# Kernel tuning notes

Measured on AMD Instinct MI355X. Metric: run time of the kernel, lower is better.

The kernel has to match this reference:

```python
import jax, jax.numpy as jnp
import numpy as np

B, T, NB, H = 1024, 128, 13, 128
T_IN = 64  # input_timesteps


def setup_inputs() -> dict:
    key = jax.random.key(0)
    ks = jax.random.split(key, 7)
    s = 1.0 / np.sqrt(H)
    return {
        "x": jax.random.normal(ks[0], (B, T, NB), dtype=jnp.float32),
        "W_ih": jax.random.normal(ks[1], (4 * H, NB), dtype=jnp.float32) * s,
        "W_hh": jax.random.normal(ks[2], (4 * H, H), dtype=jnp.float32) * s,
        "b_ih": jax.random.normal(ks[3], (4 * H,), dtype=jnp.float32) * s,
        "b_hh": jax.random.normal(ks[4], (4 * H,), dtype=jnp.float32) * s,
        "W_out": jax.random.normal(ks[5], (NB, H), dtype=jnp.float32) * s,
        "b_out": jax.random.normal(ks[6], (NB,), dtype=jnp.float32) * s,
    }


def _lstm_cell(x_t, h, c, W_ih, W_hh, b_ih, b_hh):
    # PyTorch nn.LSTM gate order: input, forget, cell(g), output
    gates = x_t @ W_ih.T + h @ W_hh.T + (b_ih + b_hh)  # [B, 4H]
    i, f, g, o = jnp.split(gates, 4, axis=-1)
    i = jax.nn.sigmoid(i)
    f = jax.nn.sigmoid(f)
    g = jnp.tanh(g)
    o = jax.nn.sigmoid(o)
    c_new = f * c + i * g
    h_new = o * jnp.tanh(c_new)
    return h_new, c_new


def reference(x, W_ih, W_hh, b_ih, b_hh, W_out, b_out):
    # forward_train with teacher_forcing=False, gp_enabled=False:
    # 1) teacher-fed LSTM over x[:, :T_IN]
    batch = x.shape[0]
    h0 = jnp.zeros((batch, H), dtype=x.dtype)
    c0 = jnp.zeros((batch, H), dtype=x.dtype)

    def step_teacher(carry, x_t):
        h, c = carry
        h, c = _lstm_cell(x_t, h, c, W_ih, W_hh, b_ih, b_hh)
        y = h @ W_out.T + b_out  # [B, NB]
        return (h, c), y

    (h, c), ys1 = jax.lax.scan(step_teacher, (h0, c0),
                               jnp.swapaxes(x[:, :T_IN], 0, 1))  # ys1: [T_IN, B, NB]

    remaining = T - T_IN - 1

    def step_auto(carry, _):
        h, c, inp = carry
        h, c = _lstm_cell(inp, h, c, W_ih, W_hh, b_ih, b_hh)
        y = h @ W_out.T + b_out
        return (h, c, y), y

    _, ys2 = jax.lax.scan(step_auto, (h, c, x[:, T_IN]), None, length=remaining)

    out = jnp.concatenate([
        x[:, 0:1],
        jnp.swapaxes(ys1, 0, 1),
        jnp.swapaxes(ys2, 0, 1),
    ], axis=1)  # [B, T, NB]
    return out
```

## Files before the change

### kernel.cpp

```cpp
#include <hip/hip_runtime.h>
#include <math.h>

#define BATCH 1024
#define TT    128
#define NBI   13
#define HH    128
#define T_INP 64
#define BB    16
#define NBLK  (BATCH/BB)

#define LOG2E 1.4426950408889634f

typedef _Float16 half8 __attribute__((ext_vector_type(8)));
typedef _Float16 half4 __attribute__((ext_vector_type(4)));
typedef float    f32x4 __attribute__((ext_vector_type(4)));

__device__ __forceinline__ unsigned short f16b(float v) {
    return __builtin_bit_cast(unsigned short, (_Float16)v);
}
__device__ __forceinline__ float rcpf_(float x) { return __builtin_amdgcn_rcpf(x); }

#if __has_builtin(__builtin_amdgcn_exp2f)
__device__ __forceinline__ float exp2_(float x) { return __builtin_amdgcn_exp2f(x); }
#else
__device__ __forceinline__ float exp2_(float x) { return __expf(x * 0.6931471805599453f); }
#endif

__device__ __forceinline__ void barrier_lds() {
    asm volatile("s_waitcnt lgkmcnt(0)" ::: "memory");
    __builtin_amdgcn_sched_barrier(0);
    __builtin_amdgcn_s_barrier();
    __builtin_amdgcn_sched_barrier(0);
}

#define WS_WHH   0
#define WS_WHAT  131072
#define WS_WIHP  262144
#define WS_WOUT  294912
#define WS_BT    299008
#define WS_BA    301056

__global__ void fold_kernel(const float* __restrict__ W_ih,
                            const float* __restrict__ W_hh,
                            const float* __restrict__ b_ih,
                            const float* __restrict__ b_hh,
                            const float* __restrict__ W_out,
                            const float* __restrict__ b_out,
                            unsigned char* __restrict__ ws)
{
    const int j = blockIdx.x;
    const int k = threadIdx.x;
    unsigned short* whh16  = (unsigned short*)(ws + WS_WHH);
    unsigned short* what16 = (unsigned short*)(ws + WS_WHAT);
    unsigned short* wihp16 = (unsigned short*)(ws + WS_WIHP);
    unsigned short* wout16 = (unsigned short*)(ws + WS_WOUT);
    float* bias_t = (float*)(ws + WS_BT);
    float* bias_a = (float*)(ws + WS_BA);

    const int gate = j >> 7;
    const float sc = (gate == 2) ? (2.0f * LOG2E) : (-LOG2E);

    float whh = W_hh[j * HH + k];
    float acc = whh;
#pragma unroll
    for (int m = 0; m < NBI; ++m)
        acc += W_ih[j * NBI + m] * W_out[m * HH + k];
    whh16[j * HH + k]  = f16b(sc * whh);
    what16[j * HH + k] = f16b(sc * acc);

    if (k < 32) wihp16[j * 32 + k] = (k < NBI) ? f16b(sc * W_ih[j * NBI + k]) : (unsigned short)0;
    if (k == 0) {
        float bt = b_ih[j] + b_hh[j];
        bias_t[j] = sc * bt;
        float ba = bt;
#pragma unroll
        for (int m = 0; m < NBI; ++m) ba += W_ih[j * NBI + m] * b_out[m];
        bias_a[j] = sc * ba;
    }
    if (j < 16) wout16[j * HH + k] = (j < NBI) ? f16b(W_out[j * HH + k]) : (unsigned short)0;
}

#define MFMA16(A, B, C) __builtin_amdgcn_mfma_f32_16x16x32_f16((A), (B), (C), 0, 0, 0)

__global__ __launch_bounds__(512, 2)
void lstm_main(const float* __restrict__ x,
               const float* __restrict__ b_out,
               const unsigned char* __restrict__ ws,
               float* __restrict__ out)
{
    const int j  = threadIdx.x;
    const int w  = j >> 6;
    const int l  = j & 63;
    const int g  = l >> 4;
    const int cb = l & 15;
    const int bbase = blockIdx.x * BB;

    const unsigned short* whh16  = (const unsigned short*)(ws + WS_WHH);
    const unsigned short* what16 = (const unsigned short*)(ws + WS_WHAT);
    const unsigned short* wihp16 = (const unsigned short*)(ws + WS_WIHP);
    const unsigned short* wout16 = (const unsigned short*)(ws + WS_WOUT);
    const float* btfp = (const float*)(ws + WS_BT);
    const float* bafp = (const float*)(ws + WS_BA);

    __shared__ half8 h_s[2][16][16];
    __shared__ half8 x_s[2][4][16];

    half8 wf[4][4];
    half8 wxf[4];
    half8 wof[4];
    f32x4 binit[4];
#pragma unroll
    for (int gate = 0; gate < 4; ++gate) {
        const int row = 128 * gate + 16 * w + cb;
#pragma unroll
        for (int kk = 0; kk < 4; ++kk)
            wf[gate][kk] = *(const half8*)(whh16 + row * HH + 32 * kk + 8 * g);
        wxf[gate] = *(const half8*)(wihp16 + row * 32 + 8 * g);
#pragma unroll
        for (int r = 0; r < 4; ++r)
            binit[gate][r] = btfp[128 * gate + 16 * w + 4 * g + r];
    }
    const bool projw = (w == 7);
#pragma unroll
    for (int kk = 0; kk < 4; ++kk)
        wof[kk] = *(const half8*)(wout16 + cb * HH + 32 * kk + 8 * g);

    float bo[4];
#pragma unroll
    for (int r = 0; r < 4; ++r) {
        const int m = 4 * g + r;
        bo[r] = (m < NBI) ? b_out[m] : 0.0f;
    }
    float* pob = out + (size_t)(bbase + cb) * TT * NBI + 4 * g;

    if (j < 256) h_s[0][j >> 4][j & 15] = (half8)(_Float16)0.0f;
    if (j < 128) ((half8*)x_s)[j] = (half8)(_Float16)0.0f;
    __syncthreads();

    int sb = 0, sm = 0;
    const float* xb = x;
    const bool do_x = (j < 208);
    float xv_hold = 0.0f, xv_pref = 0.0f;
    if (do_x) {
        sb = j / NBI; sm = j - NBI * sb;
        xb = x + (size_t)(bbase + sb) * TT * NBI + sm;
        float v = xb[0];
        ((_Float16*)&x_s[0][sm >> 3][sb])[sm & 7] = (_Float16)v;
        out[(size_t)(bbase + sb) * TT * NBI + sm] = v;
        xv_hold = xb[NBI];
    }
    __syncthreads();

    f32x4 c = {0.f, 0.f, 0.f, 0.f};
    int cur = 0;

    for (int t = 0; t <= T_INP; ++t) {
        const int nxt = cur ^ 1;

        if (do_x && t + 2 <= T_INP) xv_pref = xb[(t + 2) * NBI];

        f32x4 acc0 = binit[0], acc1 = binit[1], acc2 = binit[2], acc3 = binit[3];
        {
            half8 xf = x_s[cur][g][cb];
            acc0 = MFMA16(wxf[0], xf, acc0);
            acc1 = MFMA16(wxf[1], xf, acc1);
            acc2 = MFMA16(wxf[2], xf, acc2);
            acc3 = MFMA16(wxf[3], xf, acc3);
        }
        f32x4 pacc = {0.f, 0.f, 0.f, 0.f};
#pragma unroll
        for (int kk = 0; kk < 4; ++kk) {
            half8 hb = h_s[cur][4 * kk + g][cb];
            acc0 = MFMA16(wf[0][kk], hb, acc0);
            acc1 = MFMA16(wf[1][kk], hb, acc1);
            acc2 = MFMA16(wf[2][kk], hb, acc2);
            acc3 = MFMA16(wf[3][kk], hb, acc3);
            if (projw) pacc = MFMA16(wof[kk], hb, pacc);
        }

        half4 h4v;
#pragma unroll
        for (int r = 0; r < 4; ++r) {
            float ig = rcpf_(1.0f + exp2_(acc0[r]));
            float fg = rcpf_(1.0f + exp2_(acc1[r]));
            float eg = exp2_(acc2[r]);
            float gg = 1.0f - 2.0f * rcpf_(eg + 1.0f);
            float og = rcpf_(1.0f + exp2_(acc3[r]));
            float cn = fg * c[r] + ig * gg;
            c[r] = cn;
            float ec = exp2_(cn * 2.8853900817779268f);
            h4v[r] = (_Float16)(og * (1.0f - 2.0f * rcpf_(ec + 1.0f)));
        }
        {
            _Float16* hp = (_Float16*)&h_s[nxt][2 * w + (g >> 1)][cb];
            *(half4*)(hp + 4 * (g & 1)) = h4v;
        }
        if (do_x && t + 1 <= T_INP) {
            ((_Float16*)&x_s[nxt][sm >> 3][sb])[sm & 7] = (_Float16)xv_hold;
            xv_hold = xv_pref;
        }
        if (projw && t >= 1) {
#pragma unroll
            for (int r = 0; r < 4; ++r)
                if (4 * g + r < NBI) pob[t * NBI + r] = pacc[r] + bo[r];
        }
        barrier_lds();
        cur = nxt;
    }

#pragma unroll
    for (int gate = 0; gate < 4; ++gate) {
        const int row = 128 * gate + 16 * w + cb;
#pragma unroll
        for (int kk = 0; kk < 4; ++kk)
            wf[gate][kk] = *(const half8*)(what16 + row * HH + 32 * kk + 8 * g);
#pragma unroll
        for (int r = 0; r < 4; ++r)
            binit[gate][r] = bafp[128 * gate + 16 * w + 4 * g + r];
    }

    for (int t = T_INP + 1; t < TT - 1; ++t) {
        const int nxt = cur ^ 1;

        f32x4 acc0 = binit[0], acc1 = binit[1], acc2 = binit[2], acc3 = binit[3];
        f32x4 pacc = {0.f, 0.f, 0.f, 0.f};
#pragma unroll
        for (int kk = 0; kk < 4; ++kk) {
            half8 hb = h_s[cur][4 * kk + g][cb];
            acc0 = MFMA16(wf[0][kk], hb, acc0);
            acc1 = MFMA16(wf[1][kk], hb, acc1);
            acc2 = MFMA16(wf[2][kk], hb, acc2);
            acc3 = MFMA16(wf[3][kk], hb, acc3);
            if (projw) pacc = MFMA16(wof[kk], hb, pacc);
        }

        half4 h4v;
#pragma unroll
        for (int r = 0; r < 4; ++r) {
            float ig = rcpf_(1.0f + exp2_(acc0[r]));
            float fg = rcpf_(1.0f + exp2_(acc1[r]));
            float eg = exp2_(acc2[r]);
            float gg = 1.0f - 2.0f * rcpf_(eg + 1.0f);
            float og = rcpf_(1.0f + exp2_(acc3[r]));
            float cn = fg * c[r] + ig * gg;
            c[r] = cn;
            float ec = exp2_(cn * 2.8853900817779268f);
            h4v[r] = (_Float16)(og * (1.0f - 2.0f * rcpf_(ec + 1.0f)));
        }
        {
            _Float16* hp = (_Float16*)&h_s[nxt][2 * w + (g >> 1)][cb];
            *(half4*)(hp + 4 * (g & 1)) = h4v;
        }
        if (projw) {
#pragma unroll
            for (int r = 0; r < 4; ++r)
                if (4 * g + r < NBI) pob[t * NBI + r] = pacc[r] + bo[r];
        }
        barrier_lds();
        cur = nxt;
    }

    if (projw) {
        f32x4 pacc = {0.f, 0.f, 0.f, 0.f};
#pragma unroll
        for (int kk = 0; kk < 4; ++kk) {
            half8 hb = h_s[cur][4 * kk + g][cb];
            pacc = MFMA16(wof[kk], hb, pacc);
        }
#pragma unroll
        for (int r = 0; r < 4; ++r)
            if (4 * g + r < NBI) pob[(TT - 1) * NBI + r] = pacc[r] + bo[r];
    }
}

extern "C" void kernel_launch(void* const* d_in, const int* in_sizes, int n_in,
                              void* d_out, int out_size, void* d_ws, size_t ws_size,
                              hipStream_t stream)
{
    const float* x     = (const float*)d_in[0];
    const float* W_ih  = (const float*)d_in[1];
    const float* W_hh  = (const float*)d_in[2];
    const float* b_ih  = (const float*)d_in[3];
    const float* b_hh  = (const float*)d_in[4];
    const float* W_out = (const float*)d_in[5];
    const float* b_out = (const float*)d_in[6];
    float* out = (float*)d_out;
    unsigned char* ws = (unsigned char*)d_ws;

    fold_kernel<<<512, HH, 0, stream>>>(W_ih, W_hh, b_ih, b_hh, W_out, b_out, ws);
    lstm_main<<<NBLK, 512, 0, stream>>>(x, b_out, ws, out);
}
```

Baseline: 186.4 us.

## Stage projection outputs in LDS and flush coalesced float4 stores every four steps

Per-step output projections were written straight to global memory by one wave as scattered scalar stores. They now go into a double-buffered LDS tile and are flushed every four timesteps by 208 threads using contiguous float4 stores. The x prefetch now loads two features per thread and writes them as packed half pairs. The tanh scaling is folded into the g-gate constants, and all h loads are hoisted ahead of the MFMAs. This adds LDS traffic and flush work inside the serial recurrence loop.

```diff
diff --git a/kernel.cpp b/kernel.cpp
--- a/kernel.cpp
+++ b/kernel.cpp
@@ -10,6 +10,8 @@
 #define NBLK  (BATCH/BB)
 
 #define LOG2E 1.4426950408889634f
+#define C2L   2.8853900817779268f
+#define C4L   5.7707801635558537f
 
 typedef _Float16 half8 __attribute__((ext_vector_type(8)));
 typedef _Float16 half4 __attribute__((ext_vector_type(4)));
@@ -104,6 +106,8 @@
 
     __shared__ half8 h_s[2][16][16];
     __shared__ half8 x_s[2][4][16];
+    __shared__ float o_s[2][4][16][16];
+    float* o_sf = &o_s[0][0][0][0];
 
     half8 wf[4][4];
     half8 wxf[4];
@@ -125,29 +129,61 @@
     for (int kk = 0; kk < 4; ++kk)
         wof[kk] = *(const half8*)(wout16 + cb * HH + 32 * kk + 8 * g);
 
-    float bo[4];
+    f32x4 bo4;
 #pragma unroll
     for (int r = 0; r < 4; ++r) {
         const int m = 4 * g + r;
-        bo[r] = (m < NBI) ? b_out[m] : 0.0f;
-    }
-    float* pob = out + (size_t)(bbase + cb) * TT * NBI + 4 * g;
+        bo4[r] = (m < NBI) ? b_out[m] : 0.0f;
+    }
+    const f32x4 z4 = {0.f, 0.f, 0.f, 0.f};
+
+    const bool fl_act = (j < 208);
+    int floff0 = 0, floff1 = 0, floff2 = 0, floff3 = 0;
+    float* fgout = out;
+    if (fl_act) {
+        const int fb = j / 13, fq = j - 13 * fb;
+        fgout = out + (size_t)(bbase + fb) * TT * NBI + 4 * fq;
+#pragma unroll
+        for (int i = 0; i < 4; ++i) {
+            int s = 4 * fq + i;
+            int tr = (s >= 39) ? 3 : (s >= 26) ? 2 : (s >= 13) ? 1 : 0;
+            int m  = s - 13 * tr;
+            int off = (tr * 16 + fb) * 16 + m;
+            if (i == 0) floff0 = off; else if (i == 1) floff1 = off;
+            else if (i == 2) floff2 = off; else floff3 = off;
+        }
+    }
+#define FLUSH(FBUF, T0) do { if (fl_act) {                      \
+        float4 fv;                                              \
+        fv.x = o_sf[(FBUF) * 1024 + floff0];                    \
+        fv.y = o_sf[(FBUF) * 1024 + floff1];                    \
+        fv.z = o_sf[(FBUF) * 1024 + floff2];                    \
+        fv.w = o_sf[(FBUF) * 1024 + floff3];                    \
+        *(float4*)(fgout + (T0) * NBI) = fv; } } while (0)
+
+    const int  pidx = j - 256;
+    const bool pair = (pidx >= 0) && (pidx < 112);
+    const float* xp0 = x;
+    unsigned x_woff = 0;
+    int psix = 0;
+    float xa_h = 0.f, xb_h = 0.f, xa_p = 0.f, xb_p = 0.f;
 
     if (j < 256) h_s[0][j >> 4][j & 15] = (half8)(_Float16)0.0f;
     if (j < 128) ((half8*)x_s)[j] = (half8)(_Float16)0.0f;
-    __syncthreads();
-
-    int sb = 0, sm = 0;
-    const float* xb = x;
-    const bool do_x = (j < 208);
-    float xv_hold = 0.0f, xv_pref = 0.0f;
-    if (do_x) {
-        sb = j / NBI; sm = j - NBI * sb;
-        xb = x + (size_t)(bbase + sb) * TT * NBI + sm;
-        float v = xb[0];
-        ((_Float16*)&x_s[0][sm >> 3][sb])[sm & 7] = (_Float16)v;
-        out[(size_t)(bbase + sb) * TT * NBI + sm] = v;
-        xv_hold = xb[NBI];
+    if (pair) {
+        const int sb = pidx / 7, p = pidx - 7 * sb;
+        const int m0 = (p < 6) ? 2 * p : 12;
+        psix = (p == 6);
+        xp0 = x + (size_t)(bbase + sb) * TT * NBI + m0;
+        x_woff = (unsigned)((((m0 >> 3) * 16 + sb) * 16 + (m0 & 7) * 2));
+        float v0 = xp0[0];
+        float v1 = psix ? 0.0f : xp0[1];
+        unsigned pk = (unsigned)f16b(v0) | ((unsigned)f16b(v1) << 16);
+        *(unsigned*)((char*)&x_s[0][0][0] + x_woff) = pk;
+        o_s[0][0][sb][m0] = v0;
+        if (!psix) o_s[0][0][sb][m0 + 1] = v1;
+        xa_h = xp0[NBI];
+        xb_h = psix ? 0.0f : xp0[NBI + 1];
     }
     __syncthreads();
 
@@ -157,25 +193,38 @@
     for (int t = 0; t <= T_INP; ++t) {
         const int nxt = cur ^ 1;
 
-        if (do_x && t + 2 <= T_INP) xv_pref = xb[(t + 2) * NBI];
-
-        f32x4 acc0 = binit[0], acc1 = binit[1], acc2 = binit[2], acc3 = binit[3];
-        {
-            half8 xf = x_s[cur][g][cb];
-            acc0 = MFMA16(wxf[0], xf, acc0);
-            acc1 = MFMA16(wxf[1], xf, acc1);
-            acc2 = MFMA16(wxf[2], xf, acc2);
-            acc3 = MFMA16(wxf[3], xf, acc3);
-        }
-        f32x4 pacc = {0.f, 0.f, 0.f, 0.f};
-#pragma unroll
-        for (int kk = 0; kk < 4; ++kk) {
-            half8 hb = h_s[cur][4 * kk + g][cb];
-            acc0 = MFMA16(wf[0][kk], hb, acc0);
-            acc1 = MFMA16(wf[1][kk], hb, acc1);
-            acc2 = MFMA16(wf[2][kk], hb, acc2);
-            acc3 = MFMA16(wf[3][kk], hb, acc3);
-            if (projw) pacc = MFMA16(wof[kk], hb, pacc);
+        if ((t & 3) == 0 && t) FLUSH(((t >> 2) - 1) & 1, t - 4);
+
+        if (pair && t + 2 <= T_INP) {
+            xa_p = xp0[(t + 2) * NBI];
+            xb_p = psix ? 0.0f : xp0[(t + 2) * NBI + 1];
+        }
+
+        half8 xf  = x_s[cur][g][cb];
+        half8 hb0 = h_s[cur][g][cb];
+        half8 hb1 = h_s[cur][4 + g][cb];
+        half8 hb2 = h_s[cur][8 + g][cb];
+        half8 hb3 = h_s[cur][12 + g][cb];
+
+        f32x4 acc0 = MFMA16(wxf[0], xf, binit[0]);
+        f32x4 acc1 = MFMA16(wxf[1], xf, binit[1]);
+        f32x4 acc2 = MFMA16(wxf[2], xf, binit[2]);
+        f32x4 acc3 = MFMA16(wxf[3], xf, binit[3]);
+        acc0 = MFMA16(wf[0][0], hb0, acc0); acc1 = MFMA16(wf[1][0], hb0, acc1);
+        acc2 = MFMA16(wf[2][0], hb0, acc2); acc3 = MFMA16(wf[3][0], hb0, acc3);
+        acc0 = MFMA16(wf[0][1], hb1, acc0); acc1 = MFMA16(wf[1][1], hb1, acc1);
+        acc2 = MFMA16(wf[2][1], hb1, acc2); acc3 = MFMA16(wf[3][1], hb1, acc3);
+        acc0 = MFMA16(wf[0][2], hb2, acc0); acc1 = MFMA16(wf[1][2], hb2, acc1);
+        acc2 = MFMA16(wf[2][2], hb2, acc2); acc3 = MFMA16(wf[3][2], hb2, acc3);
+        acc0 = MFMA16(wf[0][3], hb3, acc0); acc1 = MFMA16(wf[1][3], hb3, acc1);
+        acc2 = MFMA16(wf[2][3], hb3, acc2); acc3 = MFMA16(wf[3][3], hb3, acc3);
+
+        f32x4 pacc = z4;
+        if (projw) {
+            pacc = MFMA16(wof[0], hb0, z4);
+            pacc = MFMA16(wof[1], hb1, pacc);
+            pacc = MFMA16(wof[2], hb2, pacc);
+            pacc = MFMA16(wof[3], hb3, pacc);
         }
 
         half4 h4v;
@@ -183,27 +232,26 @@
         for (int r = 0; r < 4; ++r) {
             float ig = rcpf_(1.0f + exp2_(acc0[r]));
             float fg = rcpf_(1.0f + exp2_(acc1[r]));
-            float eg = exp2_(acc2[r]);
-            float gg = 1.0f - 2.0f * rcpf_(eg + 1.0f);
+            float rg = rcpf_(exp2_(acc2[r]) + 1.0f);
+            float gp = C2L - C4L * rg;
             float og = rcpf_(1.0f + exp2_(acc3[r]));
-            float cn = fg * c[r] + ig * gg;
+            float cn = fg * c[r] + ig * gp;
             c[r] = cn;
-            float ec = exp2_(cn * 2.8853900817779268f);
+            float ec = exp2_(cn);
             h4v[r] = (_Float16)(og * (1.0f - 2.0f * rcpf_(ec + 1.0f)));
         }
         {
             _Float16* hp = (_Float16*)&h_s[nxt][2 * w + (g >> 1)][cb];
             *(half4*)(hp + 4 * (g & 1)) = h4v;
         }
-        if (do_x && t + 1 <= T_INP) {
-            ((_Float16*)&x_s[nxt][sm >> 3][sb])[sm & 7] = (_Float16)xv_hold;
-            xv_hold = xv_pref;
-        }
-        if (projw && t >= 1) {
-#pragma unroll
-            for (int r = 0; r < 4; ++r)
-                if (4 * g + r < NBI) pob[t * NBI + r] = pacc[r] + bo[r];
-        }
+        if (pair && t + 1 <= T_INP) {
+            unsigned pk = (unsigned)f16b(xa_h) | ((unsigned)f16b(xb_h) << 16);
+            *(unsigned*)((char*)&x_s[nxt][0][0] + x_woff) = pk;
+            xa_h = xa_p; xb_h = xb_p;
+        }
+        if (projw && t >= 1)
+            *(f32x4*)&o_s[(t >> 2) & 1][t & 3][cb][4 * g] = pacc + bo4;
+
         barrier_lds();
         cur = nxt;
     }
@@ -222,16 +270,30 @@
     for (int t = T_INP + 1; t < TT - 1; ++t) {
         const int nxt = cur ^ 1;
 
-        f32x4 acc0 = binit[0], acc1 = binit[1], acc2 = binit[2], acc3 = binit[3];
-        f32x4 pacc = {0.f, 0.f, 0.f, 0.f};
-#pragma unroll
-        for (int kk = 0; kk < 4; ++kk) {
-            half8 hb = h_s[cur][4 * kk + g][cb];
-            acc0 = MFMA16(wf[0][kk], hb, acc0);
-            acc1 = MFMA16(wf[1][kk], hb, acc1);
-            acc2 = MFMA16(wf[2][kk], hb, acc2);
-            acc3 = MFMA16(wf[3][kk], hb, acc3);
-            if (projw) pacc = MFMA16(wof[kk], hb, pacc);
+        if ((t & 3) == 0) FLUSH(((t >> 2) - 1) & 1, t - 4);
+
+        half8 hb0 = h_s[cur][g][cb];
+        half8 hb1 = h_s[cur][4 + g][cb];
+        half8 hb2 = h_s[cur][8 + g][cb];
+        half8 hb3 = h_s[cur][12 + g][cb];
+
+        f32x4 acc0 = MFMA16(wf[0][0], hb0, binit[0]);
+        f32x4 acc1 = MFMA16(wf[1][0], hb0, binit[1]);
+        f32x4 acc2 = MFMA16(wf[2][0], hb0, binit[2]);
+        f32x4 acc3 = MFMA16(wf[3][0], hb0, binit[3]);
+        acc0 = MFMA16(wf[0][1], hb1, acc0); acc1 = MFMA16(wf[1][1], hb1, acc1);
+        acc2 = MFMA16(wf[2][1], hb1, acc2); acc3 = MFMA16(wf[3][1], hb1, acc3);
+        acc0 = MFMA16(wf[0][2], hb2, acc0); acc1 = MFMA16(wf[1][2], hb2, acc1);
+        acc2 = MFMA16(wf[2][2], hb2, acc2); acc3 = MFMA16(wf[3][2], hb2, acc3);
+        acc0 = MFMA16(wf[0][3], hb3, acc0); acc1 = MFMA16(wf[1][3], hb3, acc1);
+        acc2 = MFMA16(wf[2][3], hb3, acc2); acc3 = MFMA16(wf[3][3], hb3, acc3);
+
+        f32x4 pacc = z4;
+        if (projw) {
+            pacc = MFMA16(wof[0], hb0, z4);
+            pacc = MFMA16(wof[1], hb1, pacc);
+            pacc = MFMA16(wof[2], hb2, pacc);
+            pacc = MFMA16(wof[3], hb3, pacc);
         }
 
         half4 h4v;
@@ -239,38 +301,39 @@
         for (int r = 0; r < 4; ++r) {
             float ig = rcpf_(1.0f + exp2_(acc0[r]));
             float fg = rcpf_(1.0f + exp2_(acc1[r]));
-            float eg = exp2_(acc2[r]);
-            float gg = 1.0f - 2.0f * rcpf_(eg + 1.0f);
+            float rg = rcpf_(exp2_(acc2[r]) + 1.0f);
+            float gp = C2L - C4L * rg;
             float og = rcpf_(1.0f + exp2_(acc3[r]));
-            float cn = fg * c[r] + ig * gg;
+            float cn = fg * c[r] + ig * gp;
             c[r] = cn;
-            float ec = exp2_(cn * 2.8853900817779268f);
+            float ec = exp2_(cn);
             h4v[r] = (_Float16)(og * (1.0f - 2.0f * rcpf_(ec + 1.0f)));
         }
         {
             _Float16* hp = (_Float16*)&h_s[nxt][2 * w + (g >> 1)][cb];
             *(half4*)(hp + 4 * (g & 1)) = h4v;
         }
-        if (projw) {
-#pragma unroll
-            for (int r = 0; r < 4; ++r)
-                if (4 * g + r < NBI) pob[t * NBI + r] = pacc[r] + bo[r];
-        }
+        if (projw)
+            *(f32x4*)&o_s[(t >> 2) & 1][t & 3][cb][4 * g] = pacc + bo4;
+
         barrier_lds();
         cur = nxt;
     }
 
     if (projw) {
-        f32x4 pacc = {0.f, 0.f, 0.f, 0.f};
-#pragma unroll
-        for (int kk = 0; kk < 4; ++kk) {
-            half8 hb = h_s[cur][4 * kk + g][cb];
-            pacc = MFMA16(wof[kk], hb, pacc);
-        }
-#pragma unroll
-        for (int r = 0; r < 4; ++r)
-            if (4 * g + r < NBI) pob[(TT - 1) * NBI + r] = pacc[r] + bo[r];
-    }
+        half8 hb0 = h_s[cur][g][cb];
+        half8 hb1 = h_s[cur][4 + g][cb];
+        half8 hb2 = h_s[cur][8 + g][cb];
+        half8 hb3 = h_s[cur][12 + g][cb];
+        f32x4 pacc = MFMA16(wof[0], hb0, z4);
+        pacc = MFMA16(wof[1], hb1, pacc);
+        pacc = MFMA16(wof[2], hb2, pacc);
+        pacc = MFMA16(wof[3], hb3, pacc);
+        *(f32x4*)&o_s[1][3][cb][4 * g] = pacc + bo4;
+    }
+    barrier_lds();
+    FLUSH(1, 124);
+#undef FLUSH
 }
 
 extern "C" void kernel_launch(void* const* d_in, const int* in_sizes, int n_in,
```

After: 179.0 us. -4.0%, faster.

## Shrink batch tile to 4 rows and split gate activation across all threads via LDS

Applied to the files above, without the earlier changes.

Reduces rows per block from 16 to 4, so the grid grows from 64 to 256 blocks and more CUs take part in the sequential recurrence. Pre-activations for the 4 valid columns are staged in a new shared float buffer after an extra barrier. Each of the 512 threads then computes the nonlinearity for a single (hidden unit, row) pair instead of 4 values per lane. The cost is a second barrier per timestep, extra LDS traffic, and 12 of 16 MFMA columns now computing padding.

```diff
diff --git a/kernel.cpp b/kernel.cpp
--- a/kernel.cpp
+++ b/kernel.cpp
@@ -6,13 +6,14 @@
 #define NBI   13
 #define HH    128
 #define T_INP 64
-#define BB    16
+#define BB    4
 #define NBLK  (BATCH/BB)
 
 #define LOG2E 1.4426950408889634f
+#define C2L   2.8853900817779268f
+#define C4L   5.7707801635558537f
 
 typedef _Float16 half8 __attribute__((ext_vector_type(8)));
-typedef _Float16 half4 __attribute__((ext_vector_type(4)));
 typedef float    f32x4 __attribute__((ext_vector_type(4)));
 
 __device__ __forceinline__ unsigned short f16b(float v) {
@@ -91,7 +92,7 @@
     const int j  = threadIdx.x;
     const int w  = j >> 6;
     const int l  = j & 63;
-    const int g  = l >> 4;
+    const int q  = l >> 4;
     const int cb = l & 15;
     const int bbase = blockIdx.x * BB;
 
@@ -104,172 +105,220 @@
 
     __shared__ half8 h_s[2][16][16];
     __shared__ half8 x_s[2][4][16];
+    __shared__ float g_sf[4 * 512];
 
     half8 wf[4][4];
     half8 wxf[4];
     half8 wof[4];
     f32x4 binit[4];
 #pragma unroll
-    for (int gate = 0; gate < 4; ++gate) {
-        const int row = 128 * gate + 16 * w + cb;
+    for (int a = 0; a < 4; ++a) {
+        const int row = 64 * w + 16 * a + cb;
 #pragma unroll
         for (int kk = 0; kk < 4; ++kk)
-            wf[gate][kk] = *(const half8*)(whh16 + row * HH + 32 * kk + 8 * g);
-        wxf[gate] = *(const half8*)(wihp16 + row * 32 + 8 * g);
+            wf[a][kk] = *(const half8*)(whh16 + row * HH + 32 * kk + 8 * q);
+        wxf[a] = *(const half8*)(wihp16 + row * 32 + 8 * q);
 #pragma unroll
         for (int r = 0; r < 4; ++r)
-            binit[gate][r] = btfp[128 * gate + 16 * w + 4 * g + r];
+            binit[a][r] = btfp[64 * w + 16 * a + 4 * q + r];
     }
     const bool projw = (w == 7);
 #pragma unroll
     for (int kk = 0; kk < 4; ++kk)
-        wof[kk] = *(const half8*)(wout16 + cb * HH + 32 * kk + 8 * g);
-
-    float bo[4];
+        wof[kk] = *(const half8*)(wout16 + cb * HH + 32 * kk + 8 * q);
+
+    f32x4 bo4;
 #pragma unroll
     for (int r = 0; r < 4; ++r) {
-        const int m = 4 * g + r;
-        bo[r] = (m < NBI) ? b_out[m] : 0.0f;
-    }
-    float* pob = out + (size_t)(bbase + cb) * TT * NBI + 4 * g;
-
-    if (j < 256) h_s[0][j >> 4][j & 15] = (half8)(_Float16)0.0f;
+        const int m = 4 * q + r;
+        bo4[r] = (m < NBI) ? b_out[m] : 0.0f;
+    }
+    const f32x4 z4 = {0.f, 0.f, 0.f, 0.f};
+    float* pob = out + (size_t)(bbase + (cb & 3)) * TT * NBI;
+
+    const int uu = j & 127;
+    const int ub = j >> 7;
+    const float* gme = g_sf + ub * 512 + uu;
+
+    const int  sid = j - 384;
+    const bool stg = (sid >= 0) && (sid < 52);
+    int s_b = 0, s_m = 0;
+    const float* xp0 = x;
+    float xa_h = 0.f;
+    if (stg) { s_b = sid / 13; s_m = sid - 13 * s_b;
+               xp0 = x + (size_t)(bbase + s_b) * TT * NBI + s_m; }
+
+    ((half8*)h_s)[j] = (half8)(_Float16)0.0f;
     if (j < 128) ((half8*)x_s)[j] = (half8)(_Float16)0.0f;
     __syncthreads();
-
-    int sb = 0, sm = 0;
-    const float* xb = x;
-    const bool do_x = (j < 208);
-    float xv_hold = 0.0f, xv_pref = 0.0f;
-    if (do_x) {
-        sb = j / NBI; sm = j - NBI * sb;
-        xb = x + (size_t)(bbase + sb) * TT * NBI + sm;
-        float v = xb[0];
-        ((_Float16*)&x_s[0][sm >> 3][sb])[sm & 7] = (_Float16)v;
-        out[(size_t)(bbase + sb) * TT * NBI + sm] = v;
-        xv_hold = xb[NBI];
+    if (stg) {
+        float v = xp0[0];
+        ((_Float16*)&x_s[0][s_m >> 3][s_b])[s_m & 7] = (_Float16)v;
+        out[(size_t)(bbase + s_b) * TT * NBI + s_m] = v;
+        xa_h = xp0[NBI];
     }
     __syncthreads();
 
-    f32x4 c = {0.f, 0.f, 0.f, 0.f};
+    float c = 0.0f;
     int cur = 0;
 
     for (int t = 0; t <= T_INP; ++t) {
         const int nxt = cur ^ 1;
 
-        if (do_x && t + 2 <= T_INP) xv_pref = xb[(t + 2) * NBI];
-
-        f32x4 acc0 = binit[0], acc1 = binit[1], acc2 = binit[2], acc3 = binit[3];
+        float xa_p = 0.f;
+        if (stg && t + 2 <= T_INP) xa_p = xp0[(t + 2) * NBI];
+
+        half8 xf  = x_s[cur][q][cb];
+        half8 hb0 = h_s[cur][q][cb];
+        half8 hb1 = h_s[cur][4 + q][cb];
+        half8 hb2 = h_s[cur][8 + q][cb];
+        half8 hb3 = h_s[cur][12 + q][cb];
+
+        f32x4 a0 = MFMA16(wxf[0], xf, binit[0]);
+        f32x4 a1 = MFMA16(wxf[1], xf, binit[1]);
+        f32x4 a2 = MFMA16(wxf[2], xf, binit[2]);
+        f32x4 a3 = MFMA16(wxf[3], xf, binit[3]);
+        a0 = MFMA16(wf[0][0], hb0, a0); a1 = MFMA16(wf[1][0], hb0, a1);
+        a2 = MFMA16(wf[2][0], hb0, a2); a3 = MFMA16(wf[3][0], hb0, a3);
+        a0 = MFMA16(wf[0][1], hb1, a0); a1 = MFMA16(wf[1][1], hb1, a1);
+        a2 = MFMA16(wf[2][1], hb1, a2); a3 = MFMA16(wf[3][1], hb1, a3);
+        a0 = MFMA16(wf[0][2], hb2, a0); a1 = MFMA16(wf[1][2], hb2, a1);
+        a2 = MFMA16(wf[2][2], hb2, a2); a3 = MFMA16(wf[3][2], hb2, a3);
+        a0 = MFMA16(wf[0][3], hb3, a0); a1 = MFMA16(wf[1][3], hb3, a1);
+        a2 = MFMA16(wf[2][3], hb3, a2); a3 = MFMA16(wf[3][3], hb3, a3);
+
+        f32x4 pacc = z4;
+        if (projw) {
+            pacc = MFMA16(wof[0], hb0, z4);
+            pacc = MFMA16(wof[1], hb1, pacc);
+            pacc = MFMA16(wof[2], hb2, pacc);
+            pacc = MFMA16(wof[3], hb3, pacc);
+        }
+
+        if (cb < 4) {
+            float* gb = g_sf + cb * 512 + 64 * w + 4 * q;
+            *(f32x4*)(gb)      = a0;
+            *(f32x4*)(gb + 16) = a1;
+            *(f32x4*)(gb + 32) = a2;
+            *(f32x4*)(gb + 48) = a3;
+        }
+        if (projw && t >= 1 && cb < 4) {
+#pragma unroll
+            for (int r = 0; r < 4; ++r) {
+                const int m = 4 * q + r;
+                if (m < NBI) pob[t * NBI + m] = pacc[r] + bo4[r];
+            }
+        }
+        barrier_lds();
+
         {
-            half8 xf = x_s[cur][g][cb];
-            acc0 = MFMA16(wxf[0], xf, acc0);
-            acc1 = MFMA16(wxf[1], xf, acc1);
-            acc2 = MFMA16(wxf[2], xf, acc2);
-            acc3 = MFMA16(wxf[3], xf, acc3);
-        }
-        f32x4 pacc = {0.f, 0.f, 0.f, 0.f};
-#pragma unroll
-        for (int kk = 0; kk < 4; ++kk) {
-            half8 hb = h_s[cur][4 * kk + g][cb];
-            acc0 = MFMA16(wf[0][kk], hb, acc0);
-            acc1 = MFMA16(wf[1][kk], hb, acc1);
-            acc2 = MFMA16(wf[2][kk], hb, acc2);
-            acc3 = MFMA16(wf[3][kk], hb, acc3);
-            if (projw) pacc = MFMA16(wof[kk], hb, pacc);
-        }
-
-        half4 h4v;
-#pragma unroll
-        for (int r = 0; r < 4; ++r) {
-            float ig = rcpf_(1.0f + exp2_(acc0[r]));
-            float fg = rcpf_(1.0f + exp2_(acc1[r]));
-            float eg = exp2_(acc2[r]);
-            float gg = 1.0f - 2.0f * rcpf_(eg + 1.0f);
-            float og = rcpf_(1.0f + exp2_(acc3[r]));
-            float cn = fg * c[r] + ig * gg;
-            c[r] = cn;
-            float ec = exp2_(cn * 2.8853900817779268f);
-            h4v[r] = (_Float16)(og * (1.0f - 2.0f * rcpf_(ec + 1.0f)));
-        }
-        {
-            _Float16* hp = (_Float16*)&h_s[nxt][2 * w + (g >> 1)][cb];
-            *(half4*)(hp + 4 * (g & 1)) = h4v;
-        }
-        if (do_x && t + 1 <= T_INP) {
-            ((_Float16*)&x_s[nxt][sm >> 3][sb])[sm & 7] = (_Float16)xv_hold;
-            xv_hold = xv_pref;
-        }
-        if (projw && t >= 1) {
-#pragma unroll
-            for (int r = 0; r < 4; ++r)
-                if (4 * g + r < NBI) pob[t * NBI + r] = pacc[r] + bo[r];
+            float gi = gme[0], gf = gme[128], gg = gme[256], go = gme[384];
+            float ig = rcpf_(1.0f + exp2_(gi));
+            float fg = rcpf_(1.0f + exp2_(gf));
+            float rg = rcpf_(exp2_(gg) + 1.0f);
+            float gp = C2L - C4L * rg;
+            float og = rcpf_(1.0f + exp2_(go));
+            float cn = fg * c + ig * gp;
+            c = cn;
+            float ec = exp2_(cn);
+            float hv = og * (1.0f - 2.0f * rcpf_(ec + 1.0f));
+            ((_Float16*)&h_s[nxt][uu >> 3][ub])[uu & 7] = (_Float16)hv;
+        }
+        if (stg && t + 1 <= T_INP) {
+            ((_Float16*)&x_s[nxt][s_m >> 3][s_b])[s_m & 7] = (_Float16)xa_h;
+            xa_h = xa_p;
         }
         barrier_lds();
         cur = nxt;
     }
 
 #pragma unroll
-    for (int gate = 0; gate < 4; ++gate) {
-        const int row = 128 * gate + 16 * w + cb;
+    for (int a = 0; a < 4; ++a) {
+        const int row = 64 * w + 16 * a + cb;
 #pragma unroll
         for (int kk = 0; kk < 4; ++kk)
-            wf[gate][kk] = *(const half8*)(what16 + row * HH + 32 * kk + 8 * g);
+            wf[a][kk] = *(const half8*)(what16 + row * HH + 32 * kk + 8 * q);
 #pragma unroll
         for (int r = 0; r < 4; ++r)
-            binit[gate][r] = bafp[128 * gate + 16 * w + 4 * g + r];
+            binit[a][r] = bafp[64 * w + 16 * a + 4 * q + r];
     }
 
     for (int t = T_INP + 1; t < TT - 1; ++t) {
         const int nxt = cur ^ 1;
 
-        f32x4 acc0 = binit[0], acc1 = binit[1], acc2 = binit[2], acc3 = binit[3];
-        f32x4 pacc = {0.f, 0.f, 0.f, 0.f};
-#pragma unroll
-        for (int kk = 0; kk < 4; ++kk) {
-            half8 hb = h_s[cur][4 * kk + g][cb];
-            acc0 = MFMA16(wf[0][kk], hb, acc0);
-            acc1 = MFMA16(wf[1][kk], hb, acc1);
-            acc2 = MFMA16(wf[2][kk], hb, acc2);
-            acc3 = MFMA16(wf[3][kk], hb, acc3);
-            if (projw) pacc = MFMA16(wof[kk], hb, pacc);
-        }
-
-        half4 h4v;
-#pragma unroll
-        for (int r = 0; r < 4; ++r) {
-            float ig = rcpf_(1.0f + exp2_(acc0[r]));
-            float fg = rcpf_(1.0f + exp2_(acc1[r]));
-            float eg = exp2_(acc2[r]);
-            float gg = 1.0f - 2.0f * rcpf_(eg + 1.0f);
-            float og = rcpf_(1.0f + exp2_(acc3[r]));
-            float cn = fg * c[r] + ig * gg;
-            c[r] = cn;
-            float ec = exp2_(cn * 2.8853900817779268f);
-            h4v[r] = (_Float16)(og * (1.0f - 2.0f * rcpf_(ec + 1.0f)));
-        }
+        half8 hb0 = h_s[cur][q][cb];
+        half8 hb1 = h_s[cur][4 + q][cb];
+        half8 hb2 = h_s[cur][8 + q][cb];
+        half8 hb3 = h_s[cur][12 + q][cb];
+
+        f32x4 a0 = MFMA16(wf[0][0], hb0, binit[0]);
+        f32x4 a1 = MFMA16(wf[1][0], hb0, binit[1]);
+        f32x4 a2 = MFMA16(wf[2][0], hb0, binit[2]);
+        f32x4 a3 = MFMA16(wf[3][0], hb0, binit[3]);
+        a0 = MFMA16(wf[0][1], hb1, a0); a1 = MFMA16(wf[1][1], hb1, a1);
+        a2 = MFMA16(wf[2][1], hb1, a2); a3 = MFMA16(wf[3][1], hb1, a3);
+        a0 = MFMA16(wf[0][2], hb2, a0); a1 = MFMA16(wf[1][2], hb2, a1);
+        a2 = MFMA16(wf[2][2], hb2, a2); a3 = MFMA16(wf[3][2], hb2, a3);
+        a0 = MFMA16(wf[0][3], hb3, a0); a1 = MFMA16(wf[1][3], hb3, a1);
+        a2 = MFMA16(wf[2][3], hb3, a2); a3 = MFMA16(wf[3][3], hb3, a3);
+
+        f32x4 pacc = z4;
+        if (projw) {
+            pacc = MFMA16(wof[0], hb0, z4);
+            pacc = MFMA16(wof[1], hb1, pacc);
+            pacc = MFMA16(wof[2], hb2, pacc);
+            pacc = MFMA16(wof[3], hb3, pacc);
+        }
+
+        if (cb < 4) {
+            float* gb = g_sf + cb * 512 + 64 * w + 4 * q;
+            *(f32x4*)(gb)      = a0;
+            *(f32x4*)(gb + 16) = a1;
+            *(f32x4*)(gb + 32) = a2;
+            *(f32x4*)(gb + 48) = a3;
+        }
+        if (projw && cb < 4) {
+#pragma unroll
+            for (int r = 0; r < 4; ++r) {
+                const int m = 4 * q + r;
+                if (m < NBI) pob[t * NBI + m] = pacc[r] + bo4[r];
+            }
+        }
+        barrier_lds();
+
         {
-            _Float16* hp = (_Float16*)&h_s[nxt][2 * w + (g >> 1)][cb];
-            *(half4*)(hp + 4 * (g & 1)) = h4v;
-        }
-        if (projw) {
-#pragma unroll
-            for (int r = 0; r < 4; ++r)
-                if (4 * g + r < NBI) pob[t * NBI + r] = pacc[r] + bo[r];
+            float gi = gme[0], gf = gme[128], gg = gme[256], go = gme[384];
+            float ig = rcpf_(1.0f + exp2_(gi));
+            float fg = rcpf_(1.0f + exp2_(gf));
+            float rg = rcpf_(exp2_(gg) + 1.0f);
+            float gp = C2L - C4L * rg;
+            float og = rcpf_(1.0f + exp2_(go));
+            float cn = fg * c + ig * gp;
+            c = cn;
+            float ec = exp2_(cn);
+            float hv = og * (1.0f - 2.0f * rcpf_(ec + 1.0f));
+            ((_Float16*)&h_s[nxt][uu >> 3][ub])[uu & 7] = (_Float16)hv;
         }
         barrier_lds();
         cur = nxt;
     }
 
     if (projw) {
-        f32x4 pacc = {0.f, 0.f, 0.f, 0.f};
-#pragma unroll
-        for (int kk = 0; kk < 4; ++kk) {
-            half8 hb = h_s[cur][4 * kk + g][cb];
-            pacc = MFMA16(wof[kk], hb, pacc);
-        }
-#pragma unroll
-        for (int r = 0; r < 4; ++r)
-            if (4 * g + r < NBI) pob[(TT - 1) * NBI + r] = pacc[r] + bo[r];
+        half8 hb0 = h_s[cur][q][cb];
+        half8 hb1 = h_s[cur][4 + q][cb];
+        half8 hb2 = h_s[cur][8 + q][cb];
+        half8 hb3 = h_s[cur][12 + q][cb];
+        f32x4 pacc = MFMA16(wof[0], hb0, z4);
+        pacc = MFMA16(wof[1], hb1, pacc);
+        pacc = MFMA16(wof[2], hb2, pacc);
+        pacc = MFMA16(wof[3], hb3, pacc);
+        if (cb < 4) {
+#pragma unroll
+            for (int r = 0; r < 4; ++r) {
+                const int m = 4 * q + r;
+                if (m < NBI) pob[(TT - 1) * NBI + m] = pacc[r] + bo4[r];
+            }
+        }
     }
 }
 
```

Measured after the change: 179.9 us. -3.5%, faster.
